# Performance work log

Measured on AMD Instinct MI355X. Metric: run time of the kernel, lower is better.

Reference implementation:

```python
import jax, jax.numpy as jnp
import numpy as np

BN_EPS = 1e-5

def _deg_inv_sqrt(idx, n):
    deg = jax.ops.segment_sum(jnp.ones(idx.shape, jnp.float32), idx, num_segments=n)
    return jnp.where(deg > 0, 1.0 / jnp.sqrt(jnp.maximum(deg, 1.0)), 0.0)

def setup_inputs() -> dict:
    key = jax.random.key(0)
    ks = jax.random.split(key, 8)
    N, E, D, L = 50000, 500000, 128, 3
    node_ids = jax.random.randint(ks[0], (N,), 0, 343)
    src = jax.random.randint(ks[1], (E,), 0, N, dtype=jnp.int32)
    dst = jax.random.randint(ks[2], (E,), 0, N, dtype=jnp.int32)
    emb_table = jax.random.normal(ks[3], (343, D), jnp.float32)
    s = 1.0 / np.sqrt(D)
    Ws = jax.random.normal(ks[4], (L, D, D), jnp.float32) * s
    bs = jnp.zeros((L, D), jnp.float32)
    Rws = jax.random.normal(ks[5], (L, D, D), jnp.float32) * s
    Rbs = jnp.zeros((L, D), jnp.float32)
    gammas = jnp.ones((L, D), jnp.float32)
    betas = jnp.zeros((L, D), jnp.float32)
    return dict(node_ids=node_ids, src=src, dst=dst, emb_table=emb_table,
                Ws=Ws, bs=bs, Rws=Rws, Rbs=Rbs, gammas=gammas, betas=betas)

def reference(node_ids, src, dst, emb_table, Ws, bs, Rws, Rbs, gammas, betas):
    N = node_ids.shape[0]
    L = Ws.shape[0]
    # GraphConv norm='both': src side uses out-degree, dst side uses in-degree
    out_norm = _deg_inv_sqrt(src, N)  # [N]
    in_norm = _deg_inv_sqrt(dst, N)   # [N]
    x = emb_table[node_ids]           # [N, D] embedding lookup
    for l in range(L):
        # D^{-1/2} A D^{-1/2} X, then linear + bias + activation (DGL GraphConv)
        h = x * out_norm[:, None]
        agg = jax.ops.segment_sum(h[src], dst, num_segments=N) * in_norm[:, None]
        h = jax.nn.relu(agg @ Ws[l] + bs[l])
        # residual branch: activation(Linear(x)) added (dgllife GCNLayer)
        h = h + jax.nn.relu(x @ Rws[l] + Rbs[l])
        # dropout p=0 (identity), then BatchNorm1d (batch statistics)
        mu = h.mean(axis=0)
        var = h.var(axis=0)
        x = gammas[l] * (h - mu) / jnp.sqrt(var + BN_EPS) + betas[l]
    return x
```

## Files before the change

### kernel.cpp

```cpp
#include <hip/hip_runtime.h>
#include <hip/hip_bf16.h>


#define TPB 256
#define NBANK 8
#define GM 16
#define APAD 136
#define NREP 8
#define CHUNK 512
#define HSZ 12500
#define HB 32

typedef __attribute__((ext_vector_type(8))) short bf16x8;
typedef __attribute__((ext_vector_type(4))) float f32x4;

__device__ inline unsigned short f2bf(float f) {
    unsigned int u = __builtin_bit_cast(unsigned int, f);
    u += 0x7fff + ((u >> 16) & 1);
    return (unsigned short)(u >> 16);
}
__device__ inline float bf2f(unsigned short b) {
    unsigned int u = ((unsigned int)b) << 16;
    return __builtin_bit_cast(float, u);
}

__global__ void src_hist(const int* __restrict__ src, unsigned short* __restrict__ out_part,
                         int E) {
    __shared__ int cnt[HSZ];
    int t = threadIdx.x;
    int s = blockIdx.x >> 5;
    int b = blockIdx.x & (HB - 1);
    int base = s * HSZ;
    for (int j = t; j < HSZ; j += TPB) cnt[j] = 0;
    __syncthreads();
    int per = (E + HB - 1) / HB;
    int lo = b * per;
    int hi = lo + per < E ? lo + per : E;
    for (int i = lo + t; i < hi; i += TPB) {
        int v = src[i] - base;
        if ((unsigned)v < (unsigned)HSZ) atomicAdd(&cnt[v], 1);
    }
    __syncthreads();
    for (int j = t; j < HSZ; j += TPB)
        out_part[(size_t)blockIdx.x * HSZ + j] = (unsigned short)cnt[j];
}

__global__ void prep1(const int* __restrict__ node_ids, const float* __restrict__ emb,
                      unsigned short* __restrict__ x, int n32,
                      const float* __restrict__ Ws, const float* __restrict__ Rws,
                      unsigned short* __restrict__ Wt, unsigned short* __restrict__ Rwt,
                      int wtotal,
                      const int* __restrict__ dst,
                      int* __restrict__ deg_rep, int* __restrict__ rank,
                      int E, int N, int degBlocks) {
    if ((int)blockIdx.x < degBlocks) {
        int rep = blockIdx.x & (NREP - 1);
        int* dd = deg_rep + (size_t)rep * N;
        int T = degBlocks * 256;
        int t0 = blockIdx.x * 256 + threadIdx.x;
        int idx[4], dv[4];
        #pragma unroll
        for (int k = 0; k < 4; k++) {
            int i = t0 + k * T;
            idx[k] = (i < E) ? i : 0;
        }
        #pragma unroll
        for (int k = 0; k < 4; k++) dv[k] = dst[idx[k]];
        int r[4];
        #pragma unroll
        for (int k = 0; k < 4; k++)
            r[k] = (t0 + k * T < E) ? atomicAdd(&dd[dv[k]], 1) : 0;
        #pragma unroll
        for (int k = 0; k < 4; k++)
            if (t0 + k * T < E) rank[t0 + k * T] = r[k] | (rep << 24);
    } else {
        int gid = (blockIdx.x - degBlocks) * 256 + threadIdx.x;
        if (gid < n32) {
            int v = gid >> 5, c4 = gid & 31;
            int id = node_ids[v];
            float4 e = *(const float4*)&emb[id * 128 + c4 * 4];
            ushort4 o;
            o.x = f2bf(e.x); o.y = f2bf(e.y); o.z = f2bf(e.z); o.w = f2bf(e.w);
            *(ushort4*)&x[(size_t)v * 128 + c4 * 4] = o;
        }
        if (gid < wtotal) {
            int l = gid >> 14, rr = (gid >> 7) & 127, k = gid & 127;
            int sidx = l * 16384 + k * 128 + rr;
            Wt[gid]  = f2bf(Ws[sidx]);
            Rwt[gid] = f2bf(Rws[sidx]);
        }
    }
}

__global__ void scan1_norm(int* __restrict__ deg_rep,
                           const unsigned short* __restrict__ out_part,
                           float* __restrict__ out_norm, float* __restrict__ in_norm,
                           int* __restrict__ row_ptr, int* __restrict__ bsum, int n) {
    __shared__ int tmp[1024];
    int t = threadIdx.x;
    int i = blockIdx.x * 1024 + t;
    int v = 0;
    int pref[NREP];
    if (i < n) {
        int run = 0;
        #pragma unroll
        for (int r = 0; r < NREP; r++) {
            int c = deg_rep[(size_t)r * n + i];
            pref[r] = run;
            run += c;
        }
        v = run;
        int s = i / HSZ;
        int li = i - s * HSZ;
        const unsigned short* op = out_part + ((size_t)s * HB) * HSZ + li;
        int dsv = 0;
        #pragma unroll 8
        for (int r = 0; r < HB; r++) dsv += op[(size_t)r * HSZ];
        out_norm[i] = dsv > 0 ? rsqrtf((float)dsv) : 0.f;
        in_norm[i]  = v   > 0 ? rsqrtf((float)v)   : 0.f;
    }
    tmp[t] = v;
    __syncthreads();
    for (int off = 1; off < 1024; off <<= 1) {
        int add = (t >= off) ? tmp[t - off] : 0;
        __syncthreads();
        tmp[t] += add;
        __syncthreads();
    }
    int ex = tmp[t] - v;
    if (i < n) {
        row_ptr[i] = ex;
        #pragma unroll
        for (int r = 0; r < NREP; r++)
            deg_rep[(size_t)r * n + i] = pref[r] + ex;
    }
    if (t == 1023) bsum[blockIdx.x] = tmp[1023];
}

__global__ void boff_scan(const int* __restrict__ bsum, int* __restrict__ boff, int nb,
                          int2* __restrict__ col_un_pad) {
    int t = threadIdx.x;
    if (nb <= 64) {
        int orig = (t < nb) ? bsum[t] : 0;
        int v = orig;
        #pragma unroll
        for (int off = 1; off < 64; off <<= 1) {
            int u = __shfl_up(v, off);
            if (t >= off) v += u;
        }
        if (t < nb) boff[t] = v - orig;
    } else if (t == 0) {
        int run = 0;
        for (int i = 0; i < nb; i++) { boff[i] = run; run += bsum[i]; }
    }
    if (t < 8) { int2 z; z.x = 0; z.y = 0; col_un_pad[t] = z; }
}

__global__ void scatter_kernel(const int* __restrict__ src, const int* __restrict__ dst,
                               const int* __restrict__ boff,
                               const int* __restrict__ rank,
                               const float* __restrict__ out_norm,
                               const int* __restrict__ deg_rep,
                               int2* __restrict__ col_un, int E, int N, int T) {
    int t0 = blockIdx.x * blockDim.x + threadIdx.x;
    int idx[4], sv[4], dv[4], rk[4];
    #pragma unroll
    for (int k = 0; k < 4; k++) {
        int i = t0 + k * T;
        idx[k] = (i < E) ? i : 0;
    }
    #pragma unroll
    for (int k = 0; k < 4; k++) { sv[k] = src[idx[k]]; dv[k] = dst[idx[k]]; rk[k] = rank[idx[k]]; }
    int pos[4]; float nm[4];
    #pragma unroll
    for (int k = 0; k < 4; k++) {
        int rep = ((unsigned)rk[k]) >> 24;
        int lr = rk[k] & 0xFFFFFF;
        pos[k] = boff[dv[k] >> 10] + deg_rep[(size_t)rep * N + dv[k]] + lr;
        nm[k] = out_norm[sv[k]];
    }
    #pragma unroll
    for (int k = 0; k < 4; k++) {
        if (t0 + k * T < E) {
            int2 v; v.x = sv[k]; v.y = __float_as_int(nm[k]);
            col_un[pos[k]] = v;
        }
    }
}

__global__ __launch_bounds__(256, 4) void fused_layer_kernel(
    const unsigned short* __restrict__ x,
    const int* __restrict__ row_ptr, const int* __restrict__ boff,
    const int2* __restrict__ col_un,
    const float* __restrict__ in_norm,
    const unsigned short* __restrict__ Wt, const unsigned short* __restrict__ Rwt,
    const float* __restrict__ bvec, const float* __restrict__ Rbvec,
    float* __restrict__ h, float* __restrict__ stats, int nrows, int Etot) {
    __shared__ unsigned short As[GM * APAD];
    __shared__ unsigned short Xs[GM * APAD];
    __shared__ int2 Ld[CHUNK];
    __shared__ float bsum[128], bss[128];
    int tid = threadIdx.x;
    int m0 = blockIdx.x * GM;
    if (tid < 128) { bsum[tid] = 0.f; bss[tid] = 0.f; }

    {
        int node = tid >> 4;
        int part = tid & 15;
        int gnode = m0 + node;
        if (gnode >= nrows) gnode = nrows - 1;
        uint4 xv = *(const uint4*)&x[(size_t)gnode * 128 + part * 8];
        *(uint4*)&Xs[node * APAD + part * 8] = xv;
        float inv = in_norm[gnode];
        int beg = row_ptr[gnode] + boff[gnode >> 10];
        int end = (gnode == nrows - 1) ? Etot
                                       : row_ptr[gnode + 1] + boff[(gnode + 1) >> 10];
        int blkBeg = row_ptr[m0] + boff[m0 >> 10];
        int lastN = m0 + GM;
        int blkEnd = (lastN >= nrows) ? Etot : row_ptr[lastN] + boff[lastN >> 10];

        float acc[8];
        #pragma unroll
        for (int j = 0; j < 8; j++) acc[j] = 0.f;
        const unsigned short* xb = x + part * 8;

        for (int chunk = blkBeg; chunk < blkEnd; chunk += CHUNK) {
            int chunkEnd = chunk + CHUNK < blkEnd ? chunk + CHUNK : blkEnd;
            int nd = chunkEnd - chunk;
            __syncthreads();
            for (int i = tid; i < nd; i += TPB) Ld[i] = col_un[chunk + i];
            __syncthreads();
            int e0 = beg > chunk ? beg : chunk;
            int e1 = end < chunkEnd ? end : chunkEnd;
            for (int e = e0; e < e1; e += 8) {
                int rem = e1 - e;
                int base = e - chunk;
                int2 ed[8];
                #pragma unroll
                for (int j = 0; j < 8; j++)
                    ed[j] = Ld[(j < rem) ? (base + j) : base];
                uint4 q[8];
                #pragma unroll
                for (int j = 0; j < 8; j++)
                    q[j] = *(const uint4*)(xb + (size_t)(unsigned)ed[j].x * 128);
                #pragma unroll
                for (int j = 0; j < 8; j++) {
                    float nn = (j < rem) ? __int_as_float(ed[j].y) : 0.f;
                    const unsigned int* w = (const unsigned int*)&q[j];
                    #pragma unroll
                    for (int t = 0; t < 4; t++) {
                        acc[2 * t]     += nn * bf2f((unsigned short)w[t]);
                        acc[2 * t + 1] += nn * bf2f((unsigned short)(w[t] >> 16));
                    }
                }
            }
        }
        #pragma unroll
        for (int j = 0; j < 8; j++) acc[j] *= inv;
        uint4 pk;
        pk.x = (unsigned int)f2bf(acc[0]) | ((unsigned int)f2bf(acc[1]) << 16);
        pk.y = (unsigned int)f2bf(acc[2]) | ((unsigned int)f2bf(acc[3]) << 16);
        pk.z = (unsigned int)f2bf(acc[4]) | ((unsigned int)f2bf(acc[5]) << 16);
        pk.w = (unsigned int)f2bf(acc[6]) | ((unsigned int)f2bf(acc[7]) << 16);
        *(uint4*)&As[node * APAD + part * 8] = pk;
    }
    __syncthreads();

    int wave = tid >> 6;
    int lane = tid & 63;
    int m = lane & 15;
    int quad = lane >> 4;

    f32x4 accA[2], accX[2];
    #pragma unroll
    for (int t = 0; t < 2; t++) { accA[t] = (f32x4){0,0,0,0}; accX[t] = (f32x4){0,0,0,0}; }

    #pragma unroll
    for (int kc = 0; kc < 4; kc++) {
        int koff = kc * 32 + quad * 8;
        bf16x8 aA = *(const bf16x8*)&As[m * APAD + koff];
        bf16x8 aX = *(const bf16x8*)&Xs[m * APAD + koff];
        #pragma unroll
        for (int t = 0; t < 2; t++) {
            int nrow = (wave * 2 + t) * 16 + m;
            bf16x8 bW = *(const bf16x8*)&Wt[(size_t)nrow * 128 + koff];
            bf16x8 bR = *(const bf16x8*)&Rwt[(size_t)nrow * 128 + koff];
            accA[t] = __builtin_amdgcn_mfma_f32_16x16x32_bf16(aA, bW, accA[t], 0, 0, 0);
            accX[t] = __builtin_amdgcn_mfma_f32_16x16x32_bf16(aX, bR, accX[t], 0, 0, 0);
        }
    }

    #pragma unroll
    for (int t = 0; t < 2; t++) {
        int col = (wave * 2 + t) * 16 + m;
        float bW = bvec[col], bR = Rbvec[col];
        float cs = 0.f, cq = 0.f;
        #pragma unroll
        for (int reg = 0; reg < 4; reg++) {
            int gr = m0 + quad * 4 + reg;
            float hA = accA[t][reg] + bW; hA = hA > 0.f ? hA : 0.f;
            float hX = accX[t][reg] + bR; hX = hX > 0.f ? hX : 0.f;
            float v = hA + hX;
            if (gr < nrows) {
                h[(size_t)gr * 128 + col] = v;
            } else {
                v = 0.f;
            }
            cs += v; cq += v * v;
        }
        cs += __shfl_xor(cs, 16); cs += __shfl_xor(cs, 32);
        cq += __shfl_xor(cq, 16); cq += __shfl_xor(cq, 32);
        if (lane < 16) {
            atomicAdd(&bsum[col], cs);
            atomicAdd(&bss[col], cq);
        }
    }
    __syncthreads();
    if (tid < 128) {
        float* sb = stats + (size_t)(blockIdx.x & (NBANK - 1)) * 256;
        atomicAdd(&sb[tid], bsum[tid]);
        atomicAdd(&sb[tid + 128], bss[tid]);
    }
}


__global__ void norm_apply_bf16(const float* __restrict__ h, const float* __restrict__ stats,
                                const float* __restrict__ gamma, const float* __restrict__ beta,
                                unsigned short* __restrict__ dstp, int total4, float n) {
    __shared__ float ssc[128], ssh[128];
    int t = threadIdx.x;
    if (t < 128) {
        float s = 0.f, sq = 0.f;
        #pragma unroll
        for (int b2 = 0; b2 < NBANK; b2++) {
            s  += stats[b2 * 256 + t];
            sq += stats[b2 * 256 + t + 128];
        }
        float mu = s / n;
        float var = sq / n - mu * mu;
        float rstd = rsqrtf(var + 1e-5f);
        float sc = gamma[t] * rstd;
        ssc[t] = sc;
        ssh[t] = beta[t] - sc * mu;
    }
    __syncthreads();
    int gid = blockIdx.x * blockDim.x + t;
    if (gid >= total4) return;
    int c4 = gid & 31;
    float4 sc = *(const float4*)&ssc[c4 * 4];
    float4 sh = *(const float4*)&ssh[c4 * 4];
    float4 v = ((const float4*)h)[gid];
    ushort4 o;
    o.x = f2bf(sc.x * v.x + sh.x);
    o.y = f2bf(sc.y * v.y + sh.y);
    o.z = f2bf(sc.z * v.z + sh.z);
    o.w = f2bf(sc.w * v.w + sh.w);
    ((ushort4*)dstp)[gid] = o;
}

__global__ void norm_apply_f32(const float* __restrict__ h, const float* __restrict__ stats,
                               const float* __restrict__ gamma, const float* __restrict__ beta,
                               float* __restrict__ dstp, int total4, float n) {
    __shared__ float ssc[128], ssh[128];
    int t = threadIdx.x;
    if (t < 128) {
        float s = 0.f, sq = 0.f;
        #pragma unroll
        for (int b2 = 0; b2 < NBANK; b2++) {
            s  += stats[b2 * 256 + t];
            sq += stats[b2 * 256 + t + 128];
        }
        float mu = s / n;
        float var = sq / n - mu * mu;
        float rstd = rsqrtf(var + 1e-5f);
        float sc = gamma[t] * rstd;
        ssc[t] = sc;
        ssh[t] = beta[t] - sc * mu;
    }
    __syncthreads();
    int gid = blockIdx.x * blockDim.x + t;
    if (gid >= total4) return;
    int c4 = gid & 31;
    float4 sc = *(const float4*)&ssc[c4 * 4];
    float4 sh = *(const float4*)&ssh[c4 * 4];
    float4 v = ((const float4*)h)[gid];
    float4 o;
    o.x = sc.x * v.x + sh.x;
    o.y = sc.y * v.y + sh.y;
    o.z = sc.z * v.z + sh.z;
    o.w = sc.w * v.w + sh.w;
    ((float4*)dstp)[gid] = o;
}


extern "C" void kernel_launch(void* const* d_in, const int* in_sizes, int n_in,
                              void* d_out, int out_size, void* d_ws, size_t ws_size,
                              hipStream_t stream) {
    const int*   node_ids = (const int*)d_in[0];
    const int*   src      = (const int*)d_in[1];
    const int*   dst      = (const int*)d_in[2];
    const float* emb      = (const float*)d_in[3];
    const float* Ws       = (const float*)d_in[4];
    const float* bs       = (const float*)d_in[5];
    const float* Rws      = (const float*)d_in[6];
    const float* Rbs      = (const float*)d_in[7];
    const float* gammas   = (const float*)d_in[8];
    const float* betas    = (const float*)d_in[9];

    const int N = in_sizes[0];
    const int E = in_sizes[1];
    const int D = 128;
    const int L = in_sizes[4] / (D * D);

    size_t off = 0;
    auto alloc = [&](size_t bytes) -> void* {
        void* p = (char*)d_ws + off;
        off += (bytes + 255) & ~(size_t)255;
        return p;
    };
    int NS = (N + HSZ - 1) / HSZ;
    int*   deg_rep  = (int*)alloc((size_t)NREP * N * 4);
    unsigned short* out_part = (unsigned short*)alloc((size_t)NS * HB * HSZ * 2);
    int*   rank     = (int*)alloc((size_t)E * 4);
    float* out_norm = (float*)alloc((size_t)N * 4);
    float* in_norm  = (float*)alloc((size_t)N * 4);
    int*   row_ptr  = (int*)alloc((size_t)(N + 1) * 4);
    int*   bsumg    = (int*)alloc(64 * 4);
    int*   boffg    = (int*)alloc(64 * 4);
    int2*  col_un   = (int2*)alloc(((size_t)E + 8) * 8);
    float* stats    = (float*)alloc((size_t)L * NBANK * 256 * 4);
    unsigned short* Wt  = (unsigned short*)alloc((size_t)L * D * D * 2);
    unsigned short* Rwt = (unsigned short*)alloc((size_t)L * D * D * 2);
    unsigned short* x   = (unsigned short*)alloc((size_t)N * D * 2);
    float* h = (float*)d_out;

    hipMemsetAsync(deg_rep, 0, (size_t)NREP * N * 4, stream);
    hipMemsetAsync(stats, 0, (size_t)L * NBANK * 256 * 4, stream);

    src_hist<<<NS * HB, TPB, 0, stream>>>(src, out_part, E);

    int degBlocks = (E + 1023) / 1024;
    int n32 = N * 32, wtotal = L * D * D;
    int embBlocks = (n32 + TPB - 1) / TPB;
    prep1<<<degBlocks + embBlocks, TPB, 0, stream>>>(
        node_ids, emb, x, n32, Ws, Rws, Wt, Rwt, wtotal,
        dst, deg_rep, rank, E, N, degBlocks);

    int nb = (N + 1023) / 1024;
    scan1_norm<<<nb, 1024, 0, stream>>>(deg_rep, out_part, out_norm, in_norm, row_ptr, bsumg, N);
    boff_scan<<<1, 64, 0, stream>>>(bsumg, boffg, nb, col_un + E);
    int scatBlocks = (E + 1023) / 1024;
    scatter_kernel<<<scatBlocks, TPB, 0, stream>>>(src, dst, boffg, rank, out_norm,
                                                   deg_rep, col_un, E, N, scatBlocks * 256);

    int gblocks = (N + GM - 1) / GM;
    for (int l = 0; l < L; l++) {
        const unsigned short* Wtl  = Wt  + (size_t)l * D * D;
        const unsigned short* Rwtl = Rwt + (size_t)l * D * D;
        const float* b   = bs  + (size_t)l * D;
        const float* Rb  = Rbs + (size_t)l * D;
        const float* gm  = gammas + (size_t)l * D;
        const float* bt  = betas  + (size_t)l * D;
        float* st = stats + (size_t)l * NBANK * 256;

        fused_layer_kernel<<<gblocks, TPB, 0, stream>>>(
            x, row_ptr, boffg, col_un, in_norm, Wtl, Rwtl, b, Rb, h, st, N, E);
        if (l < L - 1) {
            norm_apply_bf16<<<(N * 32 + TPB - 1) / TPB, TPB, 0, stream>>>(
                h, st, gm, bt, x, N * 32, (float)N);
        } else {
            norm_apply_f32<<<(N * 32 + TPB - 1) / TPB, TPB, 0, stream>>>(
                h, st, gm, bt, (float*)d_out, N * 32, (float)N);
        }
    }
}
```

Baseline: 303.8 us.

## Fold previous layer's batchnorm into next layer's gather via affine algebra

Removes the intermediate bf16 batchnorm-apply kernels by writing un-normalized layer outputs as bf16 and applying the previous layer's per-channel scale/shift inside the next fused layer kernel. The aggregation uses the identity sum(n*(a*x+b)) = a*sum(n*x) + b*sum(n), tracking the sum of edge norms per node. This saves a full read of the fp32 h and a write of x per layer, plus two kernel launches. In exchange each block recomputes the stats reduction, and the input is rounded to bf16 before normalization, which changes rounding behaviour slightly.

```diff
diff --git a/kernel.cpp b/kernel.cpp
--- a/kernel.cpp
+++ b/kernel.cpp
@@ -195,14 +195,38 @@
     const float* __restrict__ in_norm,
     const unsigned short* __restrict__ Wt, const unsigned short* __restrict__ Rwt,
     const float* __restrict__ bvec, const float* __restrict__ Rbvec,
-    float* __restrict__ h, float* __restrict__ stats, int nrows, int Etot) {
+    const float* __restrict__ prevStats, const float* __restrict__ prevGamma,
+    const float* __restrict__ prevBeta, float nrowsf,
+    float* __restrict__ h, unsigned short* __restrict__ hb,
+    float* __restrict__ stats, int nrows, int Etot) {
     __shared__ unsigned short As[GM * APAD];
     __shared__ unsigned short Xs[GM * APAD];
     __shared__ int2 Ld[CHUNK];
     __shared__ float bsum[128], bss[128];
+    __shared__ float ssc[128], ssh[128];
     int tid = threadIdx.x;
     int m0 = blockIdx.x * GM;
-    if (tid < 128) { bsum[tid] = 0.f; bss[tid] = 0.f; }
+    if (tid < 128) {
+        bsum[tid] = 0.f; bss[tid] = 0.f;
+        if (prevStats) {
+            float s = 0.f, sq = 0.f;
+            #pragma unroll
+            for (int b2 = 0; b2 < NBANK; b2++) {
+                s  += prevStats[b2 * 256 + tid];
+                sq += prevStats[b2 * 256 + tid + 128];
+            }
+            float mu = s / nrowsf;
+            float var = sq / nrowsf - mu * mu;
+            float rstd = rsqrtf(var + 1e-5f);
+            float sc = prevGamma[tid] * rstd;
+            ssc[tid] = sc;
+            ssh[tid] = prevBeta[tid] - sc * mu;
+        } else {
+            ssc[tid] = 1.f;
+            ssh[tid] = 0.f;
+        }
+    }
+    __syncthreads();
 
     {
         int node = tid >> 4;
@@ -210,7 +234,19 @@
         int gnode = m0 + node;
         if (gnode >= nrows) gnode = nrows - 1;
         uint4 xv = *(const uint4*)&x[(size_t)gnode * 128 + part * 8];
-        *(uint4*)&Xs[node * APAD + part * 8] = xv;
+        {
+            const unsigned short* xs = (const unsigned short*)&xv;
+            float c0 = ssc[part * 8 + 0], c1 = ssc[part * 8 + 1], c2 = ssc[part * 8 + 2], c3 = ssc[part * 8 + 3];
+            float c4 = ssc[part * 8 + 4], c5 = ssc[part * 8 + 5], c6 = ssc[part * 8 + 6], c7 = ssc[part * 8 + 7];
+            float d0 = ssh[part * 8 + 0], d1 = ssh[part * 8 + 1], d2 = ssh[part * 8 + 2], d3 = ssh[part * 8 + 3];
+            float d4 = ssh[part * 8 + 4], d5 = ssh[part * 8 + 5], d6 = ssh[part * 8 + 6], d7 = ssh[part * 8 + 7];
+            uint4 pk;
+            pk.x = (unsigned int)f2bf(c0 * bf2f(xs[0]) + d0) | ((unsigned int)f2bf(c1 * bf2f(xs[1]) + d1) << 16);
+            pk.y = (unsigned int)f2bf(c2 * bf2f(xs[2]) + d2) | ((unsigned int)f2bf(c3 * bf2f(xs[3]) + d3) << 16);
+            pk.z = (unsigned int)f2bf(c4 * bf2f(xs[4]) + d4) | ((unsigned int)f2bf(c5 * bf2f(xs[5]) + d5) << 16);
+            pk.w = (unsigned int)f2bf(c6 * bf2f(xs[6]) + d6) | ((unsigned int)f2bf(c7 * bf2f(xs[7]) + d7) << 16);
+            *(uint4*)&Xs[node * APAD + part * 8] = pk;
+        }
         float inv = in_norm[gnode];
         int beg = row_ptr[gnode] + boff[gnode >> 10];
         int end = (gnode == nrows - 1) ? Etot
@@ -222,6 +258,7 @@
         float acc[8];
         #pragma unroll
         for (int j = 0; j < 8; j++) acc[j] = 0.f;
+        float nsum = 0.f;
         const unsigned short* xb = x + part * 8;
 
         for (int chunk = blkBeg; chunk < blkEnd; chunk += CHUNK) {
@@ -246,6 +283,7 @@
                 #pragma unroll
                 for (int j = 0; j < 8; j++) {
                     float nn = (j < rem) ? __int_as_float(ed[j].y) : 0.f;
+                    nsum += nn;
                     const unsigned int* w = (const unsigned int*)&q[j];
                     #pragma unroll
                     for (int t = 0; t < 4; t++) {
@@ -256,7 +294,8 @@
             }
         }
         #pragma unroll
-        for (int j = 0; j < 8; j++) acc[j] *= inv;
+        for (int j = 0; j < 8; j++)
+            acc[j] = (ssc[part * 8 + j] * acc[j] + ssh[part * 8 + j] * nsum) * inv;
         uint4 pk;
         pk.x = (unsigned int)f2bf(acc[0]) | ((unsigned int)f2bf(acc[1]) << 16);
         pk.y = (unsigned int)f2bf(acc[2]) | ((unsigned int)f2bf(acc[3]) << 16);
@@ -302,7 +341,8 @@
             float hX = accX[t][reg] + bR; hX = hX > 0.f ? hX : 0.f;
             float v = hA + hX;
             if (gr < nrows) {
-                h[(size_t)gr * 128 + col] = v;
+                if (hb) hb[(size_t)gr * 128 + col] = f2bf(v);
+                else    h[(size_t)gr * 128 + col] = v;
             } else {
                 v = 0.f;
             }
@@ -321,41 +361,6 @@
         atomicAdd(&sb[tid], bsum[tid]);
         atomicAdd(&sb[tid + 128], bss[tid]);
     }
-}
-
-
-__global__ void norm_apply_bf16(const float* __restrict__ h, const float* __restrict__ stats,
-                                const float* __restrict__ gamma, const float* __restrict__ beta,
-                                unsigned short* __restrict__ dstp, int total4, float n) {
-    __shared__ float ssc[128], ssh[128];
-    int t = threadIdx.x;
-    if (t < 128) {
-        float s = 0.f, sq = 0.f;
-        #pragma unroll
-        for (int b2 = 0; b2 < NBANK; b2++) {
-            s  += stats[b2 * 256 + t];
-            sq += stats[b2 * 256 + t + 128];
-        }
-        float mu = s / n;
-        float var = sq / n - mu * mu;
-        float rstd = rsqrtf(var + 1e-5f);
-        float sc = gamma[t] * rstd;
-        ssc[t] = sc;
-        ssh[t] = beta[t] - sc * mu;
-    }
-    __syncthreads();
-    int gid = blockIdx.x * blockDim.x + t;
-    if (gid >= total4) return;
-    int c4 = gid & 31;
-    float4 sc = *(const float4*)&ssc[c4 * 4];
-    float4 sh = *(const float4*)&ssh[c4 * 4];
-    float4 v = ((const float4*)h)[gid];
-    ushort4 o;
-    o.x = f2bf(sc.x * v.x + sh.x);
-    o.y = f2bf(sc.y * v.y + sh.y);
-    o.z = f2bf(sc.z * v.z + sh.z);
-    o.w = f2bf(sc.w * v.w + sh.w);
-    ((ushort4*)dstp)[gid] = o;
 }
 
 __global__ void norm_apply_f32(const float* __restrict__ h, const float* __restrict__ stats,
@@ -429,9 +434,11 @@
     int*   boffg    = (int*)alloc(64 * 4);
     int2*  col_un   = (int2*)alloc(((size_t)E + 8) * 8);
     float* stats    = (float*)alloc((size_t)L * NBANK * 256 * 4);
-    unsigned short* Wt  = (unsigned short*)alloc((size_t)L * D * D * 2);
-    unsigned short* Rwt = (unsigned short*)alloc((size_t)L * D * D * 2);
-    unsigned short* x   = (unsigned short*)alloc((size_t)N * D * 2);
+    unsigned short* Wt   = (unsigned short*)alloc((size_t)L * D * D * 2);
+    unsigned short* Rwt  = (unsigned short*)alloc((size_t)L * D * D * 2);
+    unsigned short* x    = (unsigned short*)alloc((size_t)N * D * 2);
+    unsigned short* hb0  = (unsigned short*)alloc((size_t)N * D * 2);
+    unsigned short* hb1  = (unsigned short*)alloc((size_t)N * D * 2);
     float* h = (float*)d_out;
 
     hipMemsetAsync(deg_rep, 0, (size_t)NREP * N * 4, stream);
@@ -459,18 +466,20 @@
         const unsigned short* Rwtl = Rwt + (size_t)l * D * D;
         const float* b   = bs  + (size_t)l * D;
         const float* Rb  = Rbs + (size_t)l * D;
-        const float* gm  = gammas + (size_t)l * D;
-        const float* bt  = betas  + (size_t)l * D;
         float* st = stats + (size_t)l * NBANK * 256;
 
+        const unsigned short* xin = (l == 0) ? x : ((l & 1) ? hb0 : hb1);
+        unsigned short* hbOut = (l < L - 1) ? (((l & 1) == 0) ? hb0 : hb1) : nullptr;
+        const float* pst = (l == 0) ? nullptr : stats + (size_t)(l - 1) * NBANK * 256;
+        const float* pgm = (l == 0) ? nullptr : gammas + (size_t)(l - 1) * D;
+        const float* pbt = (l == 0) ? nullptr : betas  + (size_t)(l - 1) * D;
+
         fused_layer_kernel<<<gblocks, TPB, 0, stream>>>(
-            x, row_ptr, boffg, col_un, in_norm, Wtl, Rwtl, b, Rb, h, st, N, E);
-        if (l < L - 1) {
-            norm_apply_bf16<<<(N * 32 + TPB - 1) / TPB, TPB, 0, stream>>>(
-                h, st, gm, bt, x, N * 32, (float)N);
-        } else {
-            norm_apply_f32<<<(N * 32 + TPB - 1) / TPB, TPB, 0, stream>>>(
-                h, st, gm, bt, (float*)d_out, N * 32, (float)N);
-        }
-    }
-}
+            xin, row_ptr, boffg, col_un, in_norm, Wtl, Rwtl, b, Rb,
+            pst, pgm, pbt, (float)N, h, hbOut, st, N, E);
+    }
+    norm_apply_f32<<<(N * 32 + TPB - 1) / TPB, TPB, 0, stream>>>(
+        h, stats + (size_t)(L - 1) * NBANK * 256,
+        gammas + (size_t)(L - 1) * D, betas + (size_t)(L - 1) * D,
+        (float*)d_out, N * 32, (float)N);
+}
```

Measured after the change: 295.4 us. 2.7% less time.
